# Kernel optimization log

Measured on AMD Instinct MI355X. Metric: run time of the kernel, lower is better.

Reference implementation:

```python
import jax, jax.numpy as jnp
import numpy as np


def _sliding_window_attention(q, k, v, window_size, padding_mask):
    # q,k,v: [B,H,S,D]; faithful to the torch code incl. clamped scatter_add
    # duplicates at boundaries and the (score==0 -> -inf) quirk.
    B, H, S, D = q.shape
    hw = window_size // 2
    kp = jnp.pad(k, ((0, 0), (0, 0), (hw, hw), (0, 0)))  # zero-pad seq dim
    # window gather positions into padded keys: [S, W+1]
    pos = jnp.arange(S)[:, None] + jnp.arange(window_size + 1)[None, :]
    kw = kp[:, :, pos, :]  # [B,H,S,W+1,D]
    scores = jnp.einsum('bhsd,bhswd->bhsw', q, kw) / jnp.sqrt(jnp.asarray(D, q.dtype))
    # scatter-add into full [B,H,S,S] with clamped column indices (duplicates sum)
    idx = jnp.clip(jnp.arange(S)[:, None] + jnp.arange(-hw, hw + 1)[None, :], 0, S - 1)  # [S,W+1]
    rows = jnp.arange(S)[:, None]
    full = jnp.zeros((B, H, S, S), q.dtype).at[:, :, rows, idx].add(scores)
    neg_inf = jnp.asarray(-jnp.inf, full.dtype)
    full = jnp.where(full == 0.0, neg_inf, full)
    if padding_mask is not None:
        pm = padding_mask[:, None, None, :]  # [B,1,1,S]
        full = jnp.where(pm == 0, neg_inf, full)
        full = jnp.where(jnp.swapaxes(pm, -1, -2) == 0, neg_inf, full)
    att = jax.nn.softmax(full, axis=-1)
    att = jnp.where(jnp.isnan(att), jnp.asarray(0.0, att.dtype), att)
    values = jnp.einsum('bhst,bhtd->bhsd', att, v)
    return values, att


def setup_inputs() -> dict:
    key = jax.random.key(0)
    ks = jax.random.split(key, 5)
    B, S, IN_DIM, E = 2, 2048, 512, 512
    x = jax.random.normal(ks[0], (B, S, IN_DIM), dtype=jnp.float32)
    padding_mask = jnp.ones((B, S), dtype=jnp.int32)
    qkv_w = jax.random.normal(ks[1], (3 * E, IN_DIM), dtype=jnp.float32) * 0.02
    qkv_b = jnp.zeros((3 * E,), dtype=jnp.float32)
    o_w = jax.random.normal(ks[2], (E, E), dtype=jnp.float32) * 0.02
    o_b = jnp.zeros((E,), dtype=jnp.float32)
    return {'x': x, 'padding_mask': padding_mask, 'qkv_w': qkv_w, 'qkv_b': qkv_b,
            'o_w': o_w, 'o_b': o_b, 'window_size': 256, 'num_heads': 8}


def reference(x, padding_mask, qkv_w, qkv_b, o_w, o_b, window_size, num_heads):
    B, S, _ = x.shape
    E3 = qkv_w.shape[0]
    E = E3 // 3
    head_dim = E // num_heads
    qkv = x @ qkv_w.T + qkv_b                         # [B,S,3E]
    qkv = qkv.reshape(B, S, num_heads, 3 * head_dim)
    qkv = jnp.transpose(qkv, (0, 2, 1, 3))            # [B,H,S,3*hd]
    q, k, v = jnp.split(qkv, 3, axis=-1)
    values, _ = _sliding_window_attention(q, k, v, window_size, padding_mask)
    values = jnp.transpose(values, (0, 2, 1, 3)).reshape(B, S, E)
    o = values @ o_w.T + o_b
    return o
```

## Files before the change

### kernel.cpp

```cpp
#include <hip/hip_runtime.h>
#include <hip/hip_bf16.h>
#include <math.h>


typedef __bf16 bf16x8 __attribute__((ext_vector_type(8)));
typedef float f32x4 __attribute__((ext_vector_type(4)));

__device__ __forceinline__ unsigned short f2bf(float f) {
  unsigned u = __float_as_uint(f);
  unsigned r = u + 0x7FFFu + ((u >> 16) & 1u);
  return (unsigned short)(r >> 16);
}

__global__ __launch_bounds__(256) void cvt3_kernel(
    const float* __restrict__ s0, unsigned short* __restrict__ d0, int n0,
    const float* __restrict__ s1, unsigned short* __restrict__ d1, int n1,
    const float* __restrict__ s2, unsigned short* __restrict__ d2, int n2) {
  int i4 = blockIdx.x * 256 + threadIdx.x;
  const int c0 = n0 >> 2, c1 = (n0 + n1) >> 2, c2 = (n0 + n1 + n2) >> 2;
  const float* s; unsigned short* d; int base4;
  if (i4 < c0)      { s = s0; d = d0; base4 = i4; }
  else if (i4 < c1) { s = s1; d = d1; base4 = i4 - c0; }
  else if (i4 < c2) { s = s2; d = d2; base4 = i4 - c1; }
  else return;
  float4 v = ((const float4*)s)[base4];
  ushort4 o;
  o.x = f2bf(v.x); o.y = f2bf(v.y); o.z = f2bf(v.z); o.w = f2bf(v.w);
  ((ushort4*)d)[base4] = o;
}

__global__ __launch_bounds__(256) void gemm_qkv(
    const __hip_bfloat16* __restrict__ A, const __hip_bfloat16* __restrict__ Bw,
    const float* __restrict__ bias,
    __hip_bfloat16* __restrict__ qp, __hip_bfloat16* __restrict__ kpb,
    unsigned short* __restrict__ vtb, int M, int N, int K) {
  __shared__ __hip_bfloat16 As[128 * 40];
  __shared__ __hip_bfloat16 Bs[128 * 40];

  const int tid = threadIdx.x;
  const int wave = tid >> 6, lane = tid & 63;
  const int m0 = blockIdx.x * 128;
  const int n0 = blockIdx.y * 128;
  const int wm = (wave >> 1) * 64;
  const int wn = (wave & 1) * 64;

  f32x4 acc[4][4] = {};

  const int r0 = tid >> 2;
  const int ce = (tid & 3) * 8;
  const int row_a = wm + (lane & 15);
  const int row_b = wn + (lane & 15);
  const int ko = (lane >> 4) * 8;

  for (int k0 = 0; k0 < K; k0 += 32) {
    uint4 va0 = *(const uint4*)(A + (size_t)(m0 + r0) * K + k0 + ce);
    uint4 va1 = *(const uint4*)(A + (size_t)(m0 + 64 + r0) * K + k0 + ce);
    uint4 vb0 = *(const uint4*)(Bw + (size_t)(n0 + r0) * K + k0 + ce);
    uint4 vb1 = *(const uint4*)(Bw + (size_t)(n0 + 64 + r0) * K + k0 + ce);
    __syncthreads();
    *(uint4*)(&As[r0 * 40 + ce]) = va0;
    *(uint4*)(&As[(64 + r0) * 40 + ce]) = va1;
    *(uint4*)(&Bs[r0 * 40 + ce]) = vb0;
    *(uint4*)(&Bs[(64 + r0) * 40 + ce]) = vb1;
    __syncthreads();

    bf16x8 af[4], bf[4];
#pragma unroll
    for (int i = 0; i < 4; i++)
      af[i] = *(const bf16x8*)(&As[(row_a + i * 16) * 40 + ko]);
#pragma unroll
    for (int i = 0; i < 4; i++)
      bf[i] = *(const bf16x8*)(&Bs[(row_b + i * 16) * 40 + ko]);
#pragma unroll
    for (int mi = 0; mi < 4; mi++)
#pragma unroll
      for (int ni = 0; ni < 4; ni++)
        acc[mi][ni] = __builtin_amdgcn_mfma_f32_16x16x32_bf16(
            af[mi], bf[ni], acc[mi][ni], 0, 0, 0);
  }

  const int crow = (lane >> 4) * 4;
  const int ccol = lane & 15;
#pragma unroll
  for (int mi = 0; mi < 4; mi++) {
    const int mb = m0 + wm + mi * 16 + crow;
    const int bq = mb >> 11, sl = mb & 2047;
#pragma unroll
    for (int ni = 0; ni < 4; ni++) {
      const int n = n0 + wn + ni * 16 + ccol;
      const int h = n / 192;
      const int rem = n - h * 192;
      const int cat = rem >> 6;
      const int d = rem & 63;
      const float bv = bias[n];
      const size_t bh = (size_t)bq * 8 + h;
      if (cat == 2) {
        ushort4 o;
        o.x = f2bf(acc[mi][ni][0] + bv);
        o.y = f2bf(acc[mi][ni][1] + bv);
        o.z = f2bf(acc[mi][ni][2] + bv);
        o.w = f2bf(acc[mi][ni][3] + bv);
        *(ushort4*)(vtb + (bh * 64 + d) * 2048 + sl) = o;
      } else {
        __hip_bfloat16* dst = (cat == 0) ? qp : kpb;
        const float sc = (cat == 0) ? 0.125f : 1.0f;
#pragma unroll
        for (int r = 0; r < 4; r++)
          dst[(bh * 2048 + sl + r) * 64 + d] =
              __float2bfloat16((acc[mi][ni][r] + bv) * sc);
      }
    }
  }
}

__global__ __launch_bounds__(256) void attn_mfma(
    const __hip_bfloat16* __restrict__ qp, const __hip_bfloat16* __restrict__ kp,
    const __hip_bfloat16* __restrict__ vt, const int* __restrict__ pm,
    __hip_bfloat16* __restrict__ vals) {
  __shared__ __hip_bfloat16 sKP[320 * 72];
  __shared__ int spm[320];

  const int tid = threadIdx.x, wave = tid >> 6, lane = tid & 63;
  const int bid = blockIdx.x;
  const int s0 = (bid & 31) * 64;
  const int bh = bid >> 5;
  const int b = bh >> 3, h = bh & 7;
  const int t0 = s0 - 128;
  const int cl = lane & 15;
  const int g4 = (lane >> 4) * 4;
  const int ko = (lane >> 4) * 8;

  {
    const int e = (tid & 7) * 8;
#pragma unroll
    for (int i = 0; i < 10; i++) {
      int row = (tid >> 3) + i * 32;
      int t = t0 + row; t = min(max(t, 0), 2047);
      *(uint4*)(&sKP[row * 72 + e]) =
          *(const uint4*)(kp + ((size_t)bh * 2048 + t) * 64 + e);
    }
  }
  for (int c = tid; c < 320; c += 256) {
    int t = t0 + c;
    spm[c] = (t >= 0 && t < 2048) ? pm[b * 2048 + t] : 0;
  }
  __syncthreads();

  const __hip_bfloat16* qrow =
      qp + ((size_t)bh * 2048 + s0 + wave * 16 + cl) * 64 + ko;
  bf16x8 aq0 = *(const bf16x8*)(qrow);
  bf16x8 aq1 = *(const bf16x8*)(qrow + 32);

  f32x4 acc[17];
#pragma unroll
  for (int i = 0; i < 17; i++) {
    const int krow = (wave + i) * 16 + cl;
    bf16x8 b0 = *(const bf16x8*)(&sKP[krow * 72 + ko]);
    bf16x8 b1 = *(const bf16x8*)(&sKP[krow * 72 + ko + 32]);
    f32x4 z = {};
    z = __builtin_amdgcn_mfma_f32_16x16x32_bf16(aq0, b0, z, 0, 0, 0);
    acc[i] = __builtin_amdgcn_mfma_f32_16x16x32_bf16(aq1, b1, z, 0, 0, 0);
  }

  float mrow[4] = {-3.0e38f, -3.0e38f, -3.0e38f, -3.0e38f};
#pragma unroll
  for (int i = 0; i < 17; i++) {
    const int c = (wave + i) * 16 + cl;
    const bool cm = (spm[c] != 0);
#pragma unroll
    for (int r = 0; r < 4; r++) {
      const int qr = wave * 16 + g4 + r;
      const int dlt = c - qr;
      const bool ok = cm && dlt >= 0 && dlt <= 256;
      float sv = ok ? acc[i][r] : -3.0e38f;
      acc[i][r] = sv;
      mrow[r] = fmaxf(mrow[r], sv);
    }
  }
#pragma unroll
  for (int r = 0; r < 4; r++)
#pragma unroll
    for (int off = 1; off < 16; off <<= 1)
      mrow[r] = fmaxf(mrow[r], __shfl_xor(mrow[r], off));

  float lsum[4] = {0.f, 0.f, 0.f, 0.f};
#pragma unroll
  for (int i = 0; i < 17; i++)
#pragma unroll
    for (int r = 0; r < 4; r++) {
      float p = __expf(acc[i][r] - mrow[r]);
      acc[i][r] = p;
      lsum[r] += p;
    }
#pragma unroll
  for (int r = 0; r < 4; r++)
#pragma unroll
    for (int off = 1; off < 16; off <<= 1)
      lsum[r] += __shfl_xor(lsum[r], off);

  __syncthreads();

  __hip_bfloat16* sp = sKP + wave * 5248;
#pragma unroll
  for (int i = 0; i < 17; i++) {
    const int c = (wave + i) * 16 + cl;
#pragma unroll
    for (int r = 0; r < 4; r++)
      sp[(g4 + r) * 328 + c] = __float2bfloat16(acc[i][r]);
  }
  {
    const int zt = (wave & 1) ? (wave - 1) : (wave + 17);
    const int zc = zt * 16 + cl;
#pragma unroll
    for (int r = 0; r < 4; r++)
      sp[(g4 + r) * 328 + zc] = __float2bfloat16(0.f);
  }
  __syncthreads();

  f32x4 oacc[4] = {};
  const int k0 = wave >> 1;
  const __hip_bfloat16* vbase = vt + (size_t)bh * 64 * 2048;
#pragma unroll
  for (int ks = 0; ks < 9; ks++) {
    const int kk = (k0 + ks) * 32 + ko;
    bf16x8 pa = *(const bf16x8*)(&sp[cl * 328 + kk]);
    int tv = t0 + kk; tv = min(max(tv, 0), 2040);
#pragma unroll
    for (int ni = 0; ni < 4; ni++) {
      const int d = ni * 16 + cl;
      bf16x8 vb = *(const bf16x8*)(vbase + (size_t)d * 2048 + tv);
      oacc[ni] = __builtin_amdgcn_mfma_f32_16x16x32_bf16(pa, vb, oacc[ni], 0, 0, 0);
    }
  }

#pragma unroll
  for (int r = 0; r < 4; r++) {
    float linv = 1.0f / fmaxf(lsum[r], 1e-20f);
    const int qrow = wave * 16 + g4 + r;
    if (spm[qrow + 128] == 0) linv = 0.0f;
    const size_t obase = ((size_t)(b * 2048 + s0 + qrow)) * 512 + h * 64 + cl;
#pragma unroll
    for (int ni = 0; ni < 4; ni++)
      vals[obase + ni * 16] = __float2bfloat16(oacc[ni][r] * linv);
  }
}

__global__ __launch_bounds__(256) void gemm_out(
    const __hip_bfloat16* __restrict__ A, const __hip_bfloat16* __restrict__ Bw,
    const float* __restrict__ bias, float* __restrict__ C,
    int M, int N, int K) {
  __shared__ __hip_bfloat16 As[128 * 40];
  __shared__ __hip_bfloat16 Bs[128 * 40];

  const int tid = threadIdx.x;
  const int wave = tid >> 6, lane = tid & 63;
  const int m0 = blockIdx.x * 128;
  const int n0 = blockIdx.y * 128;
  const int wm = (wave >> 1) * 64;
  const int wn = (wave & 1) * 64;

  f32x4 acc[4][4] = {};
  const int r0 = tid >> 2;
  const int ce = (tid & 3) * 8;
  const int row_a = wm + (lane & 15);
  const int row_b = wn + (lane & 15);
  const int ko = (lane >> 4) * 8;

  for (int k0 = 0; k0 < K; k0 += 32) {
    uint4 va0 = *(const uint4*)(A + (size_t)(m0 + r0) * K + k0 + ce);
    uint4 va1 = *(const uint4*)(A + (size_t)(m0 + 64 + r0) * K + k0 + ce);
    uint4 vb0 = *(const uint4*)(Bw + (size_t)(n0 + r0) * K + k0 + ce);
    uint4 vb1 = *(const uint4*)(Bw + (size_t)(n0 + 64 + r0) * K + k0 + ce);
    __syncthreads();
    *(uint4*)(&As[r0 * 40 + ce]) = va0;
    *(uint4*)(&As[(64 + r0) * 40 + ce]) = va1;
    *(uint4*)(&Bs[r0 * 40 + ce]) = vb0;
    *(uint4*)(&Bs[(64 + r0) * 40 + ce]) = vb1;
    __syncthreads();

    bf16x8 af[4], bf[4];
#pragma unroll
    for (int i = 0; i < 4; i++)
      af[i] = *(const bf16x8*)(&As[(row_a + i * 16) * 40 + ko]);
#pragma unroll
    for (int i = 0; i < 4; i++)
      bf[i] = *(const bf16x8*)(&Bs[(row_b + i * 16) * 40 + ko]);
#pragma unroll
    for (int mi = 0; mi < 4; mi++)
#pragma unroll
      for (int ni = 0; ni < 4; ni++)
        acc[mi][ni] = __builtin_amdgcn_mfma_f32_16x16x32_bf16(
            af[mi], bf[ni], acc[mi][ni], 0, 0, 0);
  }

  const int crow = (lane >> 4) * 4;
  const int ccol = lane & 15;
#pragma unroll
  for (int mi = 0; mi < 4; mi++) {
#pragma unroll
    for (int ni = 0; ni < 4; ni++) {
      const int n = n0 + wn + ni * 16 + ccol;
      const float bv = bias[n];
      const int mb = m0 + wm + mi * 16 + crow;
#pragma unroll
      for (int r = 0; r < 4; r++)
        C[(size_t)(mb + r) * N + n] = acc[mi][ni][r] + bv;
    }
  }
}

extern "C" void kernel_launch(void* const* d_in, const int* in_sizes, int n_in,
                              void* d_out, int out_size, void* d_ws, size_t ws_size,
                              hipStream_t stream) {
  const float* x     = (const float*)d_in[0];
  const int*   pm    = (const int*)d_in[1];
  const float* qkv_w = (const float*)d_in[2];
  const float* qkv_b = (const float*)d_in[3];
  const float* o_w   = (const float*)d_in[4];
  const float* o_b   = (const float*)d_in[5];
  float* out = (float*)d_out;

  __hip_bfloat16* wsb   = (__hip_bfloat16*)d_ws;
  __hip_bfloat16* xb    = wsb;
  __hip_bfloat16* wqkvb = wsb + 2097152;
  __hip_bfloat16* wob   = wsb + 2883584;
  __hip_bfloat16* qp    = wsb + 3145728;
  __hip_bfloat16* kp    = wsb + 5242880;
  __hip_bfloat16* vt    = wsb + 7340032;
  __hip_bfloat16* vals  = wsb + 9437184;

  dim3 blk(256);
  cvt3_kernel<<<dim3(3072), blk, 0, stream>>>(
      x, (unsigned short*)xb, 2097152,
      qkv_w, (unsigned short*)wqkvb, 786432,
      o_w, (unsigned short*)wob, 262144);
  gemm_qkv<<<dim3(32, 12), blk, 0, stream>>>(
      xb, wqkvb, qkv_b, qp, kp, (unsigned short*)vt, 4096, 1536, 512);
  attn_mfma<<<dim3(512), blk, 0, stream>>>(qp, kp, vt, pm, vals);
  gemm_out<<<dim3(32, 4), blk, 0, stream>>>(vals, wob, o_b, out, 4096, 512, 512);
}
```

Measured before the change: 127.1 us.

## Use direct global-to-LDS loads in GEMMs, smaller out-GEMM tiles, cheaper softmax masking

Both GEMMs now stage A/B tiles with global_load_lds, moving data from global memory into LDS without passing through registers, and drop the padded LDS stride. The output GEMM switches to 64x128 tiles, doubling its grid for better CU occupancy. The attention kernel folds log2(e) into the Q scale so it can use exp2f, replaces the per-element window test with an additive column mask plus diagonal checks on only the first and last tiles, and stores the padding mask as float bias values. The unpadded LDS layout may cause bank conflicts on fragment reads.

```diff
diff --git a/kernel.cpp b/kernel.cpp
--- a/kernel.cpp
+++ b/kernel.cpp
@@ -10,6 +10,12 @@
   unsigned u = __float_as_uint(f);
   unsigned r = u + 0x7FFFu + ((u >> 16) & 1u);
   return (unsigned short)(r >> 16);
+}
+
+__device__ __forceinline__ void ldsdma16(void* lds, const void* g) {
+  __builtin_amdgcn_global_load_lds(
+      (const __attribute__((address_space(1))) unsigned int*)g,
+      (__attribute__((address_space(3))) unsigned int*)lds, 16, 0, 0);
 }
 
 __global__ __launch_bounds__(256) void cvt3_kernel(
@@ -33,44 +39,34 @@
     const __hip_bfloat16* __restrict__ A, const __hip_bfloat16* __restrict__ Bw,
     const float* __restrict__ bias,
     __hip_bfloat16* __restrict__ qp, __hip_bfloat16* __restrict__ kpb,
-    unsigned short* __restrict__ vtb, int M, int N, int K) {
-  __shared__ __hip_bfloat16 As[128 * 40];
-  __shared__ __hip_bfloat16 Bs[128 * 40];
-
-  const int tid = threadIdx.x;
-  const int wave = tid >> 6, lane = tid & 63;
-  const int m0 = blockIdx.x * 128;
-  const int n0 = blockIdx.y * 128;
-  const int wm = (wave >> 1) * 64;
-  const int wn = (wave & 1) * 64;
+    unsigned short* __restrict__ vtb) {
+  __shared__ __hip_bfloat16 As[128 * 32];
+  __shared__ __hip_bfloat16 Bs[128 * 32];
+
+  const int tid = threadIdx.x, wave = tid >> 6, lane = tid & 63;
+  const int m0 = blockIdx.x * 128, n0 = blockIdx.y * 128;
+  const int wm = (wave >> 1) * 64, wn = (wave & 1) * 64;
+  const int cl = lane & 15, ko = (lane >> 4) * 8;
+  const int srow = wave * 16 + (lane >> 2);
+  const int scol = (lane & 3) * 8;
 
   f32x4 acc[4][4] = {};
 
-  const int r0 = tid >> 2;
-  const int ce = (tid & 3) * 8;
-  const int row_a = wm + (lane & 15);
-  const int row_b = wn + (lane & 15);
-  const int ko = (lane >> 4) * 8;
-
-  for (int k0 = 0; k0 < K; k0 += 32) {
-    uint4 va0 = *(const uint4*)(A + (size_t)(m0 + r0) * K + k0 + ce);
-    uint4 va1 = *(const uint4*)(A + (size_t)(m0 + 64 + r0) * K + k0 + ce);
-    uint4 vb0 = *(const uint4*)(Bw + (size_t)(n0 + r0) * K + k0 + ce);
-    uint4 vb1 = *(const uint4*)(Bw + (size_t)(n0 + 64 + r0) * K + k0 + ce);
+  for (int k0 = 0; k0 < 512; k0 += 32) {
     __syncthreads();
-    *(uint4*)(&As[r0 * 40 + ce]) = va0;
-    *(uint4*)(&As[(64 + r0) * 40 + ce]) = va1;
-    *(uint4*)(&Bs[r0 * 40 + ce]) = vb0;
-    *(uint4*)(&Bs[(64 + r0) * 40 + ce]) = vb1;
+    ldsdma16(&As[wave * 512],        A  + (size_t)(m0 + srow) * 512 + k0 + scol);
+    ldsdma16(&As[2048 + wave * 512], A  + (size_t)(m0 + 64 + srow) * 512 + k0 + scol);
+    ldsdma16(&Bs[wave * 512],        Bw + (size_t)(n0 + srow) * 512 + k0 + scol);
+    ldsdma16(&Bs[2048 + wave * 512], Bw + (size_t)(n0 + 64 + srow) * 512 + k0 + scol);
     __syncthreads();
 
     bf16x8 af[4], bf[4];
 #pragma unroll
     for (int i = 0; i < 4; i++)
-      af[i] = *(const bf16x8*)(&As[(row_a + i * 16) * 40 + ko]);
+      af[i] = *(const bf16x8*)(&As[(wm + cl + i * 16) * 32 + ko]);
 #pragma unroll
     for (int i = 0; i < 4; i++)
-      bf[i] = *(const bf16x8*)(&Bs[(row_b + i * 16) * 40 + ko]);
+      bf[i] = *(const bf16x8*)(&Bs[(wn + cl + i * 16) * 32 + ko]);
 #pragma unroll
     for (int mi = 0; mi < 4; mi++)
 #pragma unroll
@@ -80,14 +76,13 @@
   }
 
   const int crow = (lane >> 4) * 4;
-  const int ccol = lane & 15;
 #pragma unroll
   for (int mi = 0; mi < 4; mi++) {
     const int mb = m0 + wm + mi * 16 + crow;
     const int bq = mb >> 11, sl = mb & 2047;
 #pragma unroll
     for (int ni = 0; ni < 4; ni++) {
-      const int n = n0 + wn + ni * 16 + ccol;
+      const int n = n0 + wn + ni * 16 + cl;
       const int h = n / 192;
       const int rem = n - h * 192;
       const int cat = rem >> 6;
@@ -103,7 +98,7 @@
         *(ushort4*)(vtb + (bh * 64 + d) * 2048 + sl) = o;
       } else {
         __hip_bfloat16* dst = (cat == 0) ? qp : kpb;
-        const float sc = (cat == 0) ? 0.125f : 1.0f;
+        const float sc = (cat == 0) ? 0.18033688011112042f : 1.0f;
 #pragma unroll
         for (int r = 0; r < 4; r++)
           dst[(bh * 2048 + sl + r) * 64 + d] =
@@ -118,7 +113,7 @@
     const __hip_bfloat16* __restrict__ vt, const int* __restrict__ pm,
     __hip_bfloat16* __restrict__ vals) {
   __shared__ __hip_bfloat16 sKP[320 * 72];
-  __shared__ int spm[320];
+  __shared__ float sCM[320];
 
   const int tid = threadIdx.x, wave = tid >> 6, lane = tid & 63;
   const int bid = blockIdx.x;
@@ -142,7 +137,8 @@
   }
   for (int c = tid; c < 320; c += 256) {
     int t = t0 + c;
-    spm[c] = (t >= 0 && t < 2048) ? pm[b * 2048 + t] : 0;
+    bool ok = (t >= 0 && t < 2048) && (pm[b * 2048 + t] != 0);
+    sCM[c] = ok ? 0.0f : -3.0e38f;
   }
   __syncthreads();
 
@@ -165,14 +161,15 @@
   float mrow[4] = {-3.0e38f, -3.0e38f, -3.0e38f, -3.0e38f};
 #pragma unroll
   for (int i = 0; i < 17; i++) {
-    const int c = (wave + i) * 16 + cl;
-    const bool cm = (spm[c] != 0);
+    const float ca = sCM[(wave + i) * 16 + cl];
 #pragma unroll
     for (int r = 0; r < 4; r++) {
-      const int qr = wave * 16 + g4 + r;
-      const int dlt = c - qr;
-      const bool ok = cm && dlt >= 0 && dlt <= 256;
-      float sv = ok ? acc[i][r] : -3.0e38f;
+      float sv = acc[i][r] + ca;
+      if (i == 0) {
+        if (cl < g4 + r) sv = -3.0e38f;
+      } else if (i == 16) {
+        if (cl > g4 + r) sv = -3.0e38f;
+      }
       acc[i][r] = sv;
       mrow[r] = fmaxf(mrow[r], sv);
     }
@@ -188,7 +185,7 @@
   for (int i = 0; i < 17; i++)
 #pragma unroll
     for (int r = 0; r < 4; r++) {
-      float p = __expf(acc[i][r] - mrow[r]);
+      float p = exp2f(acc[i][r] - mrow[r]);
       acc[i][r] = p;
       lsum[r] += p;
     }
@@ -236,9 +233,9 @@
 #pragma unroll
   for (int r = 0; r < 4; r++) {
     float linv = 1.0f / fmaxf(lsum[r], 1e-20f);
-    const int qrow = wave * 16 + g4 + r;
-    if (spm[qrow + 128] == 0) linv = 0.0f;
-    const size_t obase = ((size_t)(b * 2048 + s0 + qrow)) * 512 + h * 64 + cl;
+    const int qr = wave * 16 + g4 + r;
+    if (sCM[qr + 128] != 0.0f) linv = 0.0f;
+    const size_t obase = ((size_t)(b * 2048 + s0 + qr)) * 512 + h * 64 + cl;
 #pragma unroll
     for (int ni = 0; ni < 4; ni++)
       vals[obase + ni * 16] = __float2bfloat16(oacc[ni][r] * linv);
@@ -247,46 +244,35 @@
 
 __global__ __launch_bounds__(256) void gemm_out(
     const __hip_bfloat16* __restrict__ A, const __hip_bfloat16* __restrict__ Bw,
-    const float* __restrict__ bias, float* __restrict__ C,
-    int M, int N, int K) {
-  __shared__ __hip_bfloat16 As[128 * 40];
-  __shared__ __hip_bfloat16 Bs[128 * 40];
-
-  const int tid = threadIdx.x;
-  const int wave = tid >> 6, lane = tid & 63;
-  const int m0 = blockIdx.x * 128;
-  const int n0 = blockIdx.y * 128;
-  const int wm = (wave >> 1) * 64;
-  const int wn = (wave & 1) * 64;
-
-  f32x4 acc[4][4] = {};
-  const int r0 = tid >> 2;
-  const int ce = (tid & 3) * 8;
-  const int row_a = wm + (lane & 15);
-  const int row_b = wn + (lane & 15);
-  const int ko = (lane >> 4) * 8;
-
-  for (int k0 = 0; k0 < K; k0 += 32) {
-    uint4 va0 = *(const uint4*)(A + (size_t)(m0 + r0) * K + k0 + ce);
-    uint4 va1 = *(const uint4*)(A + (size_t)(m0 + 64 + r0) * K + k0 + ce);
-    uint4 vb0 = *(const uint4*)(Bw + (size_t)(n0 + r0) * K + k0 + ce);
-    uint4 vb1 = *(const uint4*)(Bw + (size_t)(n0 + 64 + r0) * K + k0 + ce);
+    const float* __restrict__ bias, float* __restrict__ C) {
+  __shared__ __hip_bfloat16 As[64 * 32];
+  __shared__ __hip_bfloat16 Bs[128 * 32];
+
+  const int tid = threadIdx.x, wave = tid >> 6, lane = tid & 63;
+  const int m0 = blockIdx.x * 64, n0 = blockIdx.y * 128;
+  const int wm = (wave >> 1) * 32, wn = (wave & 1) * 64;
+  const int cl = lane & 15, ko = (lane >> 4) * 8;
+  const int srow = wave * 16 + (lane >> 2);
+  const int scol = (lane & 3) * 8;
+
+  f32x4 acc[2][4] = {};
+
+  for (int k0 = 0; k0 < 512; k0 += 32) {
     __syncthreads();
-    *(uint4*)(&As[r0 * 40 + ce]) = va0;
-    *(uint4*)(&As[(64 + r0) * 40 + ce]) = va1;
-    *(uint4*)(&Bs[r0 * 40 + ce]) = vb0;
-    *(uint4*)(&Bs[(64 + r0) * 40 + ce]) = vb1;
+    ldsdma16(&As[wave * 512],        A  + (size_t)(m0 + srow) * 512 + k0 + scol);
+    ldsdma16(&Bs[wave * 512],        Bw + (size_t)(n0 + srow) * 512 + k0 + scol);
+    ldsdma16(&Bs[2048 + wave * 512], Bw + (size_t)(n0 + 64 + srow) * 512 + k0 + scol);
     __syncthreads();
 
-    bf16x8 af[4], bf[4];
+    bf16x8 af[2], bf[4];
+#pragma unroll
+    for (int i = 0; i < 2; i++)
+      af[i] = *(const bf16x8*)(&As[(wm + cl + i * 16) * 32 + ko]);
 #pragma unroll
     for (int i = 0; i < 4; i++)
-      af[i] = *(const bf16x8*)(&As[(row_a + i * 16) * 40 + ko]);
-#pragma unroll
-    for (int i = 0; i < 4; i++)
-      bf[i] = *(const bf16x8*)(&Bs[(row_b + i * 16) * 40 + ko]);
-#pragma unroll
-    for (int mi = 0; mi < 4; mi++)
+      bf[i] = *(const bf16x8*)(&Bs[(wn + cl + i * 16) * 32 + ko]);
+#pragma unroll
+    for (int mi = 0; mi < 2; mi++)
 #pragma unroll
       for (int ni = 0; ni < 4; ni++)
         acc[mi][ni] = __builtin_amdgcn_mfma_f32_16x16x32_bf16(
@@ -294,17 +280,16 @@
   }
 
   const int crow = (lane >> 4) * 4;
-  const int ccol = lane & 15;
-#pragma unroll
-  for (int mi = 0; mi < 4; mi++) {
+#pragma unroll
+  for (int mi = 0; mi < 2; mi++) {
 #pragma unroll
     for (int ni = 0; ni < 4; ni++) {
-      const int n = n0 + wn + ni * 16 + ccol;
+      const int n = n0 + wn + ni * 16 + cl;
       const float bv = bias[n];
       const int mb = m0 + wm + mi * 16 + crow;
 #pragma unroll
       for (int r = 0; r < 4; r++)
-        C[(size_t)(mb + r) * N + n] = acc[mi][ni][r] + bv;
+        C[(size_t)(mb + r) * 512 + n] = acc[mi][ni][r] + bv;
     }
   }
 }
@@ -335,7 +320,7 @@
       qkv_w, (unsigned short*)wqkvb, 786432,
       o_w, (unsigned short*)wob, 262144);
   gemm_qkv<<<dim3(32, 12), blk, 0, stream>>>(
-      xb, wqkvb, qkv_b, qp, kp, (unsigned short*)vt, 4096, 1536, 512);
+      xb, wqkvb, qkv_b, qp, kp, (unsigned short*)vt);
   attn_mfma<<<dim3(512), blk, 0, stream>>>(qp, kp, vt, pm, vals);
-  gemm_out<<<dim3(32, 4), blk, 0, stream>>>(vals, wob, o_b, out, 4096, 512, 512);
-}
+  gemm_out<<<dim3(64, 4), blk, 0, stream>>>(vals, wob, o_b, out);
+}
```

New measurement: 118.9 us. -6.5%, faster.
